# Kernel tuning notes

Measured on AMD Instinct MI355X. Metric: run time of the kernel, lower is better.

The kernel has to match this reference:

```python
import jax, jax.numpy as jnp
import numpy as np
import itertools

RADIUS = 0.1
DILATION = 0.05
KSIZE = 3
NDIM = 3
EPS = 1e-12


def _offsets():
    # 3^ndim kernel-cell offsets centered on the particle, spaced by dilation
    half = (KSIZE - 1) / 2.0
    offs = np.array(list(itertools.product(range(KSIZE), repeat=NDIM)), dtype=np.float32)
    return jnp.asarray((offs - half) * DILATION)  # [K, NDIM]


def setup_inputs() -> dict:
    key = jax.random.key(0)
    k1, k2, k3, k4, k5 = jax.random.split(key, 5)
    B, N, C, O = 2, 4096, 16, 16
    K = KSIZE ** NDIM
    locs = jax.random.uniform(k1, (B, N, NDIM), dtype=jnp.float32)
    data = jax.random.normal(k2, (B, N, C), dtype=jnp.float32)
    # densities strictly positive, bounded away from zero
    density = jax.random.uniform(k3, (B, N), dtype=jnp.float32, minval=0.5, maxval=1.5)
    weight = jax.random.normal(k4, (O, C, K), dtype=jnp.float32) * 0.1
    bias = jax.random.normal(k5, (O,), dtype=jnp.float32) * 0.01
    return {"locs": locs, "data": data, "density": density, "weight": weight, "bias": bias}


def reference(locs, data, density, weight, bias):
    # SPH continuous convolution (ConvSP):
    # out[b,i,o] = bias[o] + sum_k sum_c weight[o,c,k] *
    #              sum_j (data[b,j,c]/density[b,j]) * W(||locs[b,j] - (locs[b,i]+off_k)||)
    # with smoothing kernel W(d) = (1 - d/radius)^3 for d < radius, else 0.
    B, N, _ = locs.shape
    O = weight.shape[0]
    offs = _offsets()                                # [K, NDIM]
    wK = jnp.transpose(weight, (2, 0, 1))            # [K, O, C]
    nd = data / density[..., None]                   # [B, N, C] density-normalized features
    l2 = jnp.sum(locs * locs, axis=-1)               # [B, N]

    def step(acc, xs):
        off, wk = xs                                 # off:[NDIM], wk:[O,C]
        c = locs + off                               # shifted query centers [B,N,NDIM]
        c2 = jnp.sum(c * c, axis=-1)                 # [B,N]
        d2 = c2[:, :, None] + l2[:, None, :] - 2.0 * jnp.einsum('bid,bjd->bij', c, locs)
        d = jnp.sqrt(jnp.maximum(d2, EPS))           # [B,N,N]
        w = jnp.where(d < RADIUS, (1.0 - d / RADIUS) ** 3, 0.0)
        kv = jnp.einsum('bij,bjc->bic', w, nd)       # [B,N,C]
        return acc + jnp.einsum('bic,oc->bio', kv, wk), None

    init = jnp.zeros((B, N, O), dtype=data.dtype)
    out, _ = jax.lax.scan(jax.checkpoint(step), init, (offs, wK))
    return out + bias
```

## Files before the change

kernel.cpp:

```cpp
#include <hip/hip_runtime.h>

#define NP 4096
#define NSLAB 64
#define ZSPAN 10
#define EPS_K 1e-12f

__global__ void k_hist(const float* __restrict__ locs, int* __restrict__ cnt, int totalP) {
    int i = blockIdx.x * 256 + threadIdx.x;
    if (i < totalP) {
        float z = locs[i * 3 + 2];
        int c = min(max((int)(z * 64.0f), 0), 63);
        atomicAdd(&cnt[(i >> 12) * NSLAB + c], 1);
    }
}

__global__ void k_scan(const int* __restrict__ cnt, int* __restrict__ off, int B) {
    int lane = threadIdx.x & 63;
    int b = threadIdx.x >> 6;
    if (b >= B) return;
    int incl = cnt[b * NSLAB + lane];
    for (int d = 1; d < 64; d <<= 1) {
        int o = __shfl_up(incl, d, 64);
        if (lane >= d) incl += o;
    }
    off[b * (NSLAB + 1) + lane + 1] = incl;
    if (lane == 0) off[b * (NSLAB + 1)] = 0;
}

__global__ __launch_bounds__(256) void k_rank(const float* __restrict__ locs,
                                              const int* __restrict__ off,
                                              int* __restrict__ list) {
    int b = blockIdx.x / NSLAB;
    int s = blockIdx.x % NSLAB;
    const float* lz = locs + (size_t)b * NP * 3;
    __shared__ int wtot[4];
    int base = off[b * (NSLAB + 1) + s];
    int running = 0;
    int tid = threadIdx.x, lane = tid & 63, w = tid >> 6;
    for (int chunk = 0; chunk < NP; chunk += 256) {
        int i = chunk + tid;
        float z = lz[i * 3 + 2];
        int c = min(max((int)(z * 64.0f), 0), 63);
        bool match = (c == s);
        unsigned long long m = __ballot(match);
        int pre = __popcll(m & ((1ull << lane) - 1ull));
        if (lane == 0) wtot[w] = (int)__popcll(m);
        __syncthreads();
        int bp = 0, tot = 0;
        for (int ww = 0; ww < 4; ++ww) { if (ww < w) bp += wtot[ww]; tot += wtot[ww]; }
        if (match) list[b * NP + base + running + bp + pre] = i;
        running += tot;
        __syncthreads();
    }
}

__global__ void k_reorder(const float* __restrict__ locs, const float* __restrict__ data,
                          const float* __restrict__ density, const int* __restrict__ list,
                          float4* __restrict__ slocs, float4* __restrict__ snd, int totalP) {
    int idx = blockIdx.x * 256 + threadIdx.x;
    if (idx >= totalP * 4) return;
    int pos = idx >> 2, q = idx & 3;
    int b = pos >> 12;
    int orig = list[pos];
    float invr = 1.0f / density[(b << 12) + orig];
    const float4 dv = ((const float4*)(data))[(((size_t)(b << 12) + orig) << 2) + q];
    float4 o4 = { dv.x * invr, dv.y * invr, dv.z * invr, dv.w * invr };
    snd[idx] = o4;
    if (q == 0) {
        const float* lp = locs + ((size_t)(b << 12) + orig) * 3;
        float4 s4 = { lp[0], lp[1], lp[2], __int_as_float(orig) };
        slocs[pos] = s4;
    }
}

__global__ void k_wt(const float* __restrict__ weight, float* __restrict__ wT) {
    int idx = blockIdx.x * 256 + threadIdx.x;
    if (idx >= 27 * 256) return;
    int k = idx >> 8, oc = idx & 255;
    wT[k * 256 + oc] = weight[oc * 27 + k];
}

__global__ __launch_bounds__(256) void k_main(
    const float4* __restrict__ slocs,
    const float4* __restrict__ snd,
    const int* __restrict__ off,
    const float* __restrict__ wT,
    const float* __restrict__ bias,
    float* __restrict__ out)
{
    const int bid  = blockIdx.x;
    const int b    = bid >> 9;
    const int blk  = bid & 511;
    const int tid  = threadIdx.x;
    const int p    = tid >> 5;
    const int lane = tid & 31;

    const float4* slb  = slocs + ((size_t)b << 12);
    const float4* sndb = snd   + ((size_t)b << 14);
    const int*    offb = off + b * (NSLAB + 1);

    const int P0 = blk << 3;
    const float4 me = slb[P0 + p];
    const int orig = __float_as_int(me.w);

    const int s_lo = min(max((int)(slb[P0].z     * 64.0f), 0), 63);
    const int s_hi = min(max((int)(slb[P0 + 7].z * 64.0f), 0), 63);
    const int jstart = offb[max(s_lo - ZSPAN, 0)];
    const int jend   = offb[min(s_hi + ZSPAN, NSLAB - 1) + 1];

    float cx, cy, cz;
    {
        int kk = (lane < 27) ? lane : 13;
        cx = me.x + (float)(kk / 9       - 1) * 0.05f;
        cy = me.y + (float)((kk / 3) % 3 - 1) * 0.05f;
        cz = me.z + (float)(kk % 3       - 1) * 0.05f;
        if (lane >= 27) cx = 1e9f;
    }

    float kv[16];
#pragma unroll
    for (int c = 0; c < 16; ++c) kv[c] = 0.f;

    const int nsteps = (jend - jstart + 31) >> 5;
    int pos0 = jstart + lane;
    float4 lj = slb[min(pos0, jend - 1)];
    if (pos0 >= jend) lj.x = 1e9f;

    for (int st = 0; st < nsteps; ++st) {
        const int cbase = jstart + (st << 5);
        const int posn = cbase + 32 + lane;
        float4 ljn = slb[min(posn, jend - 1)];
        if (posn >= jend) ljn.x = 1e9f;

        const float ex = fmaxf(fabsf(me.x - lj.x) - 0.05f, 0.f);
        const float ey = fmaxf(fabsf(me.y - lj.y) - 0.05f, 0.f);
        const float ez = fmaxf(fabsf(me.z - lj.z) - 0.05f, 0.f);
        const float bd2 = ex * ex + ey * ey + ez * ez;
        unsigned int mh = (unsigned int)(__ballot(bd2 < 0.01f) >> (tid & 32));

        while (mh) {
            const int bit = __ffs(mh) - 1;
            mh &= mh - 1;
            const float4* dp = sndb + (((size_t)(cbase + bit)) << 2);
            const float4 v0 = dp[0], v1 = dp[1], v2 = dp[2], v3 = dp[3];
            const float qx = __shfl(lj.x, bit, 32);
            const float qy = __shfl(lj.y, bit, 32);
            const float qz = __shfl(lj.z, bit, 32);
            const float dx = cx - qx, dy = cy - qy, dz = cz - qz;
            const float d2 = dx * dx + dy * dy + dz * dz;
            const float d = sqrtf(fmaxf(d2, EPS_K));
            float t1 = fmaxf(__builtin_fmaf(d, -10.f, 1.f), 0.f);
            const float w = t1 * t1 * t1;
            kv[ 0] = fmaf(w, v0.x, kv[ 0]);
            kv[ 1] = fmaf(w, v0.y, kv[ 1]);
            kv[ 2] = fmaf(w, v0.z, kv[ 2]);
            kv[ 3] = fmaf(w, v0.w, kv[ 3]);
            kv[ 4] = fmaf(w, v1.x, kv[ 4]);
            kv[ 5] = fmaf(w, v1.y, kv[ 5]);
            kv[ 6] = fmaf(w, v1.z, kv[ 6]);
            kv[ 7] = fmaf(w, v1.w, kv[ 7]);
            kv[ 8] = fmaf(w, v2.x, kv[ 8]);
            kv[ 9] = fmaf(w, v2.y, kv[ 9]);
            kv[10] = fmaf(w, v2.z, kv[10]);
            kv[11] = fmaf(w, v2.w, kv[11]);
            kv[12] = fmaf(w, v3.x, kv[12]);
            kv[13] = fmaf(w, v3.y, kv[13]);
            kv[14] = fmaf(w, v3.z, kv[14]);
            kv[15] = fmaf(w, v3.w, kv[15]);
        }
        lj = ljn;
    }

    const int kk = (lane < 27) ? lane : 26;
    const float4* wrow = (const float4*)(wT + kk * 256);
    float res = 0.f;
#pragma unroll
    for (int o = 0; o < 16; ++o) {
        const float4 w0 = wrow[o * 4 + 0], w1 = wrow[o * 4 + 1];
        const float4 w2 = wrow[o * 4 + 2], w3 = wrow[o * 4 + 3];
        float acc = 0.f;
        acc = fmaf(w0.x, kv[ 0], acc); acc = fmaf(w0.y, kv[ 1], acc);
        acc = fmaf(w0.z, kv[ 2], acc); acc = fmaf(w0.w, kv[ 3], acc);
        acc = fmaf(w1.x, kv[ 4], acc); acc = fmaf(w1.y, kv[ 5], acc);
        acc = fmaf(w1.z, kv[ 6], acc); acc = fmaf(w1.w, kv[ 7], acc);
        acc = fmaf(w2.x, kv[ 8], acc); acc = fmaf(w2.y, kv[ 9], acc);
        acc = fmaf(w2.z, kv[10], acc); acc = fmaf(w2.w, kv[11], acc);
        acc = fmaf(w3.x, kv[12], acc); acc = fmaf(w3.y, kv[13], acc);
        acc = fmaf(w3.z, kv[14], acc); acc = fmaf(w3.w, kv[15], acc);
#pragma unroll
        for (int dsh = 16; dsh >= 1; dsh >>= 1)
            acc += __shfl_xor(acc, dsh, 32);
        if (lane == o) res = acc;
    }
    if (lane < 16)
        out[(((size_t)(b << 12)) + orig) * 16 + lane] = res + bias[lane];
}

extern "C" void kernel_launch(void* const* d_in, const int* in_sizes, int n_in,
                              void* d_out, int out_size, void* d_ws, size_t ws_size,
                              hipStream_t stream) {
    const float* locs    = (const float*)d_in[0];
    const float* data    = (const float*)d_in[1];
    const float* density = (const float*)d_in[2];
    const float* weight  = (const float*)d_in[3];
    const float* bias    = (const float*)d_in[4];
    float* out = (float*)d_out;

    const int B = in_sizes[2] / NP;
    const int totalP = B * NP;

    char* ws = (char*)d_ws;
    size_t o = 0;
    auto take = [&](size_t bytes) { size_t r = o; o = (o + bytes + 255) & ~(size_t)255; return r; };
    float4* slocs = (float4*)(ws + take((size_t)totalP * 16));
    float4* snd   = (float4*)(ws + take((size_t)totalP * 64));
    float*  wT    = (float*)(ws + take(27 * 256 * 4));
    int*    cnt   = (int*)(ws + take((size_t)B * NSLAB * 4));
    int*    off   = (int*)(ws + take((size_t)B * (NSLAB + 1) * 4));
    int*    list  = (int*)(ws + take((size_t)totalP * 4));

    hipMemsetAsync(cnt, 0, (size_t)B * NSLAB * 4, stream);
    k_hist<<<(totalP + 255) / 256, 256, 0, stream>>>(locs, cnt, totalP);
    k_scan<<<1, 64 * B, 0, stream>>>(cnt, off, B);
    k_rank<<<B * NSLAB, 256, 0, stream>>>(locs, off, list);
    k_reorder<<<(totalP * 4 + 255) / 256, 256, 0, stream>>>(locs, data, density, list, slocs, snd, totalP);
    k_wt<<<27, 256, 0, stream>>>(weight, wT);
    k_main<<<B * 512, 256, 0, stream>>>(slocs, snd, off, wT, bias, out);
}
```

Measured before the change: 110.7 us.

## Fuse scan/rank/reorder into atomic scatter and use per-particle wave64 neighbor search

Replaces the separate scan, rank, reorder and weight-transpose kernels with one scatter kernel. It computes slab offsets per block and places particles using atomic cursors, which cuts the launch count from six kernels to three. The main kernel now assigns one full 64-lane wave per particle with a per-particle slab window instead of an 8-particle shared window. The two half-waves split the candidate list and their kv sums are combined by shuffle. In exchange, atomic placement makes the ordering within a slab nondeterministic, and neighbor positions are reloaded from memory instead of shuffled.

```diff
diff --git a/kernel.cpp b/kernel.cpp
--- a/kernel.cpp
+++ b/kernel.cpp
@@ -14,70 +14,57 @@
     }
 }
 
-__global__ void k_scan(const int* __restrict__ cnt, int* __restrict__ off, int B) {
-    int lane = threadIdx.x & 63;
-    int b = threadIdx.x >> 6;
-    if (b >= B) return;
-    int incl = cnt[b * NSLAB + lane];
-    for (int d = 1; d < 64; d <<= 1) {
-        int o = __shfl_up(incl, d, 64);
-        if (lane >= d) incl += o;
-    }
-    off[b * (NSLAB + 1) + lane + 1] = incl;
-    if (lane == 0) off[b * (NSLAB + 1)] = 0;
-}
-
-__global__ __launch_bounds__(256) void k_rank(const float* __restrict__ locs,
-                                              const int* __restrict__ off,
-                                              int* __restrict__ list) {
-    int b = blockIdx.x / NSLAB;
-    int s = blockIdx.x % NSLAB;
-    const float* lz = locs + (size_t)b * NP * 3;
-    __shared__ int wtot[4];
-    int base = off[b * (NSLAB + 1) + s];
-    int running = 0;
-    int tid = threadIdx.x, lane = tid & 63, w = tid >> 6;
-    for (int chunk = 0; chunk < NP; chunk += 256) {
-        int i = chunk + tid;
-        float z = lz[i * 3 + 2];
-        int c = min(max((int)(z * 64.0f), 0), 63);
-        bool match = (c == s);
-        unsigned long long m = __ballot(match);
-        int pre = __popcll(m & ((1ull << lane) - 1ull));
-        if (lane == 0) wtot[w] = (int)__popcll(m);
-        __syncthreads();
-        int bp = 0, tot = 0;
-        for (int ww = 0; ww < 4; ++ww) { if (ww < w) bp += wtot[ww]; tot += wtot[ww]; }
-        if (match) list[b * NP + base + running + bp + pre] = i;
-        running += tot;
-        __syncthreads();
-    }
-}
-
-__global__ void k_reorder(const float* __restrict__ locs, const float* __restrict__ data,
-                          const float* __restrict__ density, const int* __restrict__ list,
-                          float4* __restrict__ slocs, float4* __restrict__ snd, int totalP) {
-    int idx = blockIdx.x * 256 + threadIdx.x;
-    if (idx >= totalP * 4) return;
-    int pos = idx >> 2, q = idx & 3;
-    int b = pos >> 12;
-    int orig = list[pos];
-    float invr = 1.0f / density[(b << 12) + orig];
-    const float4 dv = ((const float4*)(data))[(((size_t)(b << 12) + orig) << 2) + q];
-    float4 o4 = { dv.x * invr, dv.y * invr, dv.z * invr, dv.w * invr };
-    snd[idx] = o4;
-    if (q == 0) {
-        const float* lp = locs + ((size_t)(b << 12) + orig) * 3;
-        float4 s4 = { lp[0], lp[1], lp[2], __int_as_float(orig) };
-        slocs[pos] = s4;
-    }
-}
-
-__global__ void k_wt(const float* __restrict__ weight, float* __restrict__ wT) {
-    int idx = blockIdx.x * 256 + threadIdx.x;
-    if (idx >= 27 * 256) return;
-    int k = idx >> 8, oc = idx & 255;
-    wT[k * 256 + oc] = weight[oc * 27 + k];
+__global__ __launch_bounds__(256) void k_scatter(
+    const float* __restrict__ locs, const float* __restrict__ data,
+    const float* __restrict__ density, const float* __restrict__ weight,
+    const int* __restrict__ cnt, int* __restrict__ cursor,
+    float4* __restrict__ slocs, float4* __restrict__ snd,
+    int* __restrict__ off, float* __restrict__ wT)
+{
+    __shared__ int s_off[NSLAB + 1];
+    const int tid = threadIdx.x;
+    const int b = blockIdx.x >> 4;
+
+    if (tid < 64) {
+        int incl = cnt[b * NSLAB + tid];
+        for (int d = 1; d < 64; d <<= 1) {
+            int o = __shfl_up(incl, d, 64);
+            if (tid >= d) incl += o;
+        }
+        s_off[tid + 1] = incl;
+        if (tid == 0) s_off[0] = 0;
+    }
+    __syncthreads();
+
+    const int il = ((blockIdx.x & 15) << 8) + tid;
+    const size_t gi = ((size_t)b << 12) + il;
+    const float* lp = locs + gi * 3;
+    const float x = lp[0], y = lp[1], z = lp[2];
+    const int bin = min(max((int)(z * 64.0f), 0), 63);
+    const int r = atomicAdd(&cursor[b * NSLAB + bin], 1);
+    const int pos = s_off[bin] + r;
+    const size_t gp = ((size_t)b << 12) + pos;
+
+    float4 s4 = { x, y, z, __int_as_float(il) };
+    slocs[gp] = s4;
+    const float invr = 1.0f / density[gi];
+    const float4* dsrc = (const float4*)data + (gi << 2);
+    float4* ddst = snd + (gp << 2);
+#pragma unroll
+    for (int q = 0; q < 4; ++q) {
+        float4 v = dsrc[q];
+        float4 o4 = { v.x * invr, v.y * invr, v.z * invr, v.w * invr };
+        ddst[q] = o4;
+    }
+
+    if ((blockIdx.x & 15) == 0 && tid <= NSLAB)
+        off[b * (NSLAB + 1) + tid] = s_off[tid];
+    if (blockIdx.x == 0) {
+        for (int i2 = tid; i2 < 27 * 256; i2 += 256) {
+            int k = i2 >> 8, oc = i2 & 255;
+            wT[k * 256 + oc] = weight[oc * 27 + k];
+        }
+    }
 }
 
 __global__ __launch_bounds__(256) void k_main(
@@ -88,65 +75,65 @@
     const float* __restrict__ bias,
     float* __restrict__ out)
 {
-    const int bid  = blockIdx.x;
-    const int b    = bid >> 9;
-    const int blk  = bid & 511;
     const int tid  = threadIdx.x;
-    const int p    = tid >> 5;
-    const int lane = tid & 31;
+    const int wid  = tid >> 6;
+    const int lane = tid & 63;
+    const int hsh  = lane & 32;
+    const int l32  = lane & 31;
+
+    const int bid = blockIdx.x;
+    const int b   = bid >> 10;
+    const int p   = ((bid & 1023) << 2) + wid;
 
     const float4* slb  = slocs + ((size_t)b << 12);
     const float4* sndb = snd   + ((size_t)b << 14);
     const int*    offb = off + b * (NSLAB + 1);
 
-    const int P0 = blk << 3;
-    const float4 me = slb[P0 + p];
+    const float4 me = slb[p];
     const int orig = __float_as_int(me.w);
-
-    const int s_lo = min(max((int)(slb[P0].z     * 64.0f), 0), 63);
-    const int s_hi = min(max((int)(slb[P0 + 7].z * 64.0f), 0), 63);
-    const int jstart = offb[max(s_lo - ZSPAN, 0)];
-    const int jend   = offb[min(s_hi + ZSPAN, NSLAB - 1) + 1];
+    const int sp = min(max((int)(me.z * 64.0f), 0), 63);
+    const int jstart = offb[max(sp - ZSPAN, 0)];
+    const int jend   = offb[min(sp + ZSPAN, NSLAB - 1) + 1];
 
     float cx, cy, cz;
     {
-        int kk = (lane < 27) ? lane : 13;
+        int kk = (l32 < 27) ? l32 : 13;
         cx = me.x + (float)(kk / 9       - 1) * 0.05f;
         cy = me.y + (float)((kk / 3) % 3 - 1) * 0.05f;
         cz = me.z + (float)(kk % 3       - 1) * 0.05f;
-        if (lane >= 27) cx = 1e9f;
+        if (l32 >= 27) cx = 1e9f;
     }
 
     float kv[16];
 #pragma unroll
     for (int c = 0; c < 16; ++c) kv[c] = 0.f;
 
-    const int nsteps = (jend - jstart + 31) >> 5;
-    int pos0 = jstart + lane;
-    float4 lj = slb[min(pos0, jend - 1)];
-    if (pos0 >= jend) lj.x = 1e9f;
+    const int nsteps = (jend - jstart + 63) >> 6;
+    int idx0 = jstart + lane;
+    float4 lj = slb[min(idx0, jend - 1)];
+    if (idx0 >= jend) lj.x = 1e9f;
 
     for (int st = 0; st < nsteps; ++st) {
-        const int cbase = jstart + (st << 5);
-        const int posn = cbase + 32 + lane;
-        float4 ljn = slb[min(posn, jend - 1)];
-        if (posn >= jend) ljn.x = 1e9f;
+        const int tbase = jstart + (st << 6);
+        const int idxn = tbase + 64 + lane;
+        float4 ljn = slb[min(idxn, jend - 1)];
 
         const float ex = fmaxf(fabsf(me.x - lj.x) - 0.05f, 0.f);
         const float ey = fmaxf(fabsf(me.y - lj.y) - 0.05f, 0.f);
         const float ez = fmaxf(fabsf(me.z - lj.z) - 0.05f, 0.f);
         const float bd2 = ex * ex + ey * ey + ez * ez;
-        unsigned int mh = (unsigned int)(__ballot(bd2 < 0.01f) >> (tid & 32));
+        const unsigned long long ball = __ballot(bd2 < 0.01f);
+        unsigned int mh = (unsigned int)(ball >> hsh);
+        const int cbase = tbase + hsh;
 
         while (mh) {
             const int bit = __ffs(mh) - 1;
             mh &= mh - 1;
-            const float4* dp = sndb + (((size_t)(cbase + bit)) << 2);
+            const int j = cbase + bit;
+            const float4 q = slb[j];
+            const float4* dp = sndb + ((size_t)j << 2);
             const float4 v0 = dp[0], v1 = dp[1], v2 = dp[2], v3 = dp[3];
-            const float qx = __shfl(lj.x, bit, 32);
-            const float qy = __shfl(lj.y, bit, 32);
-            const float qz = __shfl(lj.z, bit, 32);
-            const float dx = cx - qx, dy = cy - qy, dz = cz - qz;
+            const float dx = cx - q.x, dy = cy - q.y, dz = cz - q.z;
             const float d2 = dx * dx + dy * dy + dz * dz;
             const float d = sqrtf(fmaxf(d2, EPS_K));
             float t1 = fmaxf(__builtin_fmaf(d, -10.f, 1.f), 0.f);
@@ -168,10 +155,15 @@
             kv[14] = fmaf(w, v3.z, kv[14]);
             kv[15] = fmaf(w, v3.w, kv[15]);
         }
+        if (idxn >= jend) ljn.x = 1e9f;
         lj = ljn;
     }
 
-    const int kk = (lane < 27) ? lane : 26;
+#pragma unroll
+    for (int c = 0; c < 16; ++c)
+        kv[c] += __shfl_xor(kv[c], 32, 64);
+
+    const int kk = (l32 < 27) ? l32 : 26;
     const float4* wrow = (const float4*)(wT + kk * 256);
     float res = 0.f;
 #pragma unroll
@@ -190,7 +182,7 @@
 #pragma unroll
         for (int dsh = 16; dsh >= 1; dsh >>= 1)
             acc += __shfl_xor(acc, dsh, 32);
-        if (lane == o) res = acc;
+        if (l32 == o) res = acc;
     }
     if (lane < 16)
         out[(((size_t)(b << 12)) + orig) * 16 + lane] = res + bias[lane];
@@ -212,18 +204,16 @@
     char* ws = (char*)d_ws;
     size_t o = 0;
     auto take = [&](size_t bytes) { size_t r = o; o = (o + bytes + 255) & ~(size_t)255; return r; };
-    float4* slocs = (float4*)(ws + take((size_t)totalP * 16));
-    float4* snd   = (float4*)(ws + take((size_t)totalP * 64));
-    float*  wT    = (float*)(ws + take(27 * 256 * 4));
-    int*    cnt   = (int*)(ws + take((size_t)B * NSLAB * 4));
-    int*    off   = (int*)(ws + take((size_t)B * (NSLAB + 1) * 4));
-    int*    list  = (int*)(ws + take((size_t)totalP * 4));
-
-    hipMemsetAsync(cnt, 0, (size_t)B * NSLAB * 4, stream);
+    float4* slocs  = (float4*)(ws + take((size_t)totalP * 16));
+    float4* snd    = (float4*)(ws + take((size_t)totalP * 64));
+    float*  wT     = (float*)(ws + take(27 * 256 * 4));
+    int*    cnt    = (int*)(ws + take((size_t)B * NSLAB * 4 * 2));
+    int*    cursor = cnt + B * NSLAB;
+    int*    off    = (int*)(ws + take((size_t)B * (NSLAB + 1) * 4));
+
+    hipMemsetAsync(cnt, 0, (size_t)B * NSLAB * 4 * 2, stream);
     k_hist<<<(totalP + 255) / 256, 256, 0, stream>>>(locs, cnt, totalP);
-    k_scan<<<1, 64 * B, 0, stream>>>(cnt, off, B);
-    k_rank<<<B * NSLAB, 256, 0, stream>>>(locs, off, list);
-    k_reorder<<<(totalP * 4 + 255) / 256, 256, 0, stream>>>(locs, data, density, list, slocs, snd, totalP);
-    k_wt<<<27, 256, 0, stream>>>(weight, wT);
-    k_main<<<B * 512, 256, 0, stream>>>(slocs, snd, off, wT, bias, out);
-}
+    k_scatter<<<totalP / 256, 256, 0, stream>>>(locs, data, density, weight,
+                                                cnt, cursor, slocs, snd, off, wT);
+    k_main<<<B * 1024, 256, 0, stream>>>(slocs, snd, off, wT, bias, out);
+}
```

New measurement: 150.7 us. +36.1%, slower.
